# Kernel optimization log

Hardware: AMD Instinct MI355X
Metric: run time of the kernel (lower is better)

The kernel has to match this reference:

```python
import jax, jax.numpy as jnp
import numpy as np

B, L, C, H = 2, 2048, 1024, 16  # batches, tokens per batch, channels, heads


def _ln(x, eps=1e-6):
    # LayerNorm32: no affine, eps=1e-6, computed in fp32
    x32 = x.astype(jnp.float32)
    m = x32.mean(-1, keepdims=True)
    v = ((x32 - m) ** 2).mean(-1, keepdims=True)
    return ((x32 - m) * jax.lax.rsqrt(v + eps)).astype(x.dtype)


def setup_inputs() -> dict:
    key = jax.random.key(0)
    ks = jax.random.split(key, 8)
    s = 0.02
    return {
        "feats": jax.random.normal(ks[0], (B * L, C), jnp.float32),
        "mod": jax.random.normal(ks[1], (B, C), jnp.float32),
        "w_mod": jax.random.normal(ks[2], (C, 6 * C), jnp.float32) * s,
        "b_mod": jnp.zeros((6 * C,), jnp.float32),
        "w_qkv": jax.random.normal(ks[3], (C, 3 * C), jnp.float32) * s,
        "b_qkv": jnp.zeros((3 * C,), jnp.float32),
        "w_proj": jax.random.normal(ks[4], (C, C), jnp.float32) * s,
        "b_proj": jnp.zeros((C,), jnp.float32),
        "w_fc1": jax.random.normal(ks[5], (C, 4 * C), jnp.float32) * s,
        "b_fc1": jnp.zeros((4 * C,), jnp.float32),
        "w_fc2": jax.random.normal(ks[6], (4 * C, C), jnp.float32) * s,
        "b_fc2": jnp.zeros((C,), jnp.float32),
        "seq_len": L,
    }


def reference(feats, mod, w_mod, b_mod, w_qkv, b_qkv, w_proj, b_proj,
              w_fc1, b_fc1, w_fc2, b_fc2, seq_len):
    Bn, Cn = mod.shape
    Ln = seq_len
    Hn = H
    D = Cn // Hn

    # adaLN modulation: SiLU -> Linear(C, 6C), chunk into 6 [B, C] pieces
    m = jax.nn.silu(mod) @ w_mod + b_mod
    sh_a, sc_a, g_a, sh_m, sc_m, g_m = jnp.split(m, 6, axis=1)

    x = feats.reshape(Bn, Ln, Cn)

    # --- MSA branch ---
    h = _ln(x)
    h = h * (1.0 + sc_a[:, None]) + sh_a[:, None]
    qkv = h @ w_qkv + b_qkv  # [B, L, 3C]
    q, k, v = [t.reshape(Bn, Ln, Hn, D) for t in jnp.split(qkv, 3, axis=-1)]
    scores = jnp.einsum('bqhd,bkhd->bhqk', q, k) / jnp.sqrt(jnp.float32(D))
    a = jax.nn.softmax(scores, axis=-1)
    o = jnp.einsum('bhqk,bkhd->bqhd', a, v).reshape(Bn, Ln, Cn)
    o = o @ w_proj + b_proj
    x = x + o * g_a[:, None]

    # --- FFN branch ---
    h = _ln(x)
    h = h * (1.0 + sc_m[:, None]) + sh_m[:, None]
    h = jax.nn.gelu(h @ w_fc1 + b_fc1, approximate=False) @ w_fc2 + b_fc2
    x = x + h * g_m[:, None]

    return x.reshape(Bn * Ln, Cn)
```

## Files before the change

### kernel.cpp

```cpp
#include <hip/hip_runtime.h>
#include <hip/hip_bf16.h>
#include <math.h>

#define B_ 2
#define L_ 2048
#define C_ 1024
#define H_ 16
#define D_ 64

typedef __attribute__((ext_vector_type(8))) short short8;
typedef __attribute__((ext_vector_type(4))) float float4v;

__device__ inline short f2bs(float f) {
    union { __hip_bfloat16 h; short s; } u; u.h = __float2bfloat16(f); return u.s;
}

#define GL2LDS(gp, lp)                                                         \
    __builtin_amdgcn_global_load_lds(                                          \
        (const __attribute__((address_space(1))) void*)(gp),                   \
        (__attribute__((address_space(3))) void*)(lp), 16, 0, 0)

__global__ __launch_bounds__(256) void k_mod2(const float* __restrict__ mod,
                                              const float* __restrict__ w_mod,
                                              const float* __restrict__ b_mod,
                                              float* __restrict__ m_out) {
    __shared__ float a_s[2][256];
    const int t = threadIdx.x;
    const int seg = blockIdx.y;
    for (int i = t; i < 512; i += 256) {
        float a = mod[(i >> 8) * C_ + seg * 256 + (i & 255)];
        a_s[i >> 8][i & 255] = a / (1.f + __expf(-a));
    }
    __syncthreads();
    int j = blockIdx.x * 256 + t;
    float acc0 = (seg == 0) ? b_mod[j] : 0.f;
    float acc1 = acc0;
    for (int k = 0; k < 256; ++k) {
        float w = w_mod[(size_t)(seg * 256 + k) * (6 * C_) + j];
        acc0 += a_s[0][k] * w;
        acc1 += a_s[1][k] * w;
    }
    atomicAdd(&m_out[j], acc0);
    atomicAdd(&m_out[6 * C_ + j], acc1);
}

__global__ __launch_bounds__(256) void k_wt(const float* __restrict__ W,
                                            short* __restrict__ WT,
                                            int K, int N) {
    __shared__ short T[64][72];
    const int t = threadIdx.x;
    const int n0 = blockIdx.x * 64, k0 = blockIdx.y * 64;
    {
        int kr = t >> 2, nc = (t & 3) * 16;
        const float* src = W + (size_t)(k0 + kr) * N + n0 + nc;
#pragma unroll
        for (int j = 0; j < 16; ++j) T[kr][nc + j] = f2bs(src[j]);
    }
    __syncthreads();
    {
        int nr = t >> 2, kc = (t & 3) * 16;
        short8 o0, o1;
#pragma unroll
        for (int j = 0; j < 8; ++j) { o0[j] = T[kc + j][nr]; o1[j] = T[kc + 8 + j][nr]; }
        short* dst = WT + (size_t)(n0 + nr) * K + k0 + kc;
        *(short8*)dst = o0;
        *(short8*)(dst + 8) = o1;
    }
}

__global__ __launch_bounds__(256) void k_vt(const __hip_bfloat16* __restrict__ qkv,
                                            short* __restrict__ vt) {
    __shared__ short T[64][72];
    const int t = threadIdx.x;
    const int kt = blockIdx.x * 64;
    const int bh = blockIdx.y;
    const int h = bh & (H_ - 1), b = bh >> 4;
    const __hip_bfloat16* src = qkv + ((size_t)(b * L_ + kt)) * (3 * C_) + 2 * C_ + h * D_;
    {
        int kr = t >> 2, dg = (t & 3) * 16;
        const short8* s = (const short8*)(src + (size_t)kr * (3 * C_) + dg);
        *(short8*)&T[kr][dg] = s[0];
        *(short8*)&T[kr][dg + 8] = s[1];
    }
    __syncthreads();
    {
        int dr = t >> 2, kg = (t & 3) * 16;
        short8 o0, o1;
#pragma unroll
        for (int j = 0; j < 8; ++j) { o0[j] = T[kg + j][dr]; o1[j] = T[kg + 8 + j][dr]; }
        short* dst = vt + ((size_t)bh * D_ + dr) * L_ + kt + kg;
        *(short8*)dst = o0;
        *(short8*)(dst + 8) = o1;
    }
}

__global__ __launch_bounds__(256) void k_ln_mod(const float* __restrict__ x,
                                                const float* __restrict__ mvec,
                                                int off_sh, int off_sc,
                                                __hip_bfloat16* __restrict__ h_out) {
    int row = blockIdx.x;
    int b = row / L_;
    int t = threadIdx.x;
    float v[4];
    float s = 0.f, ss = 0.f;
#pragma unroll
    for (int i = 0; i < 4; ++i) {
        int c = t + i * 256;
        float val = x[(size_t)row * C_ + c];
        v[i] = val; s += val; ss += val * val;
    }
#pragma unroll
    for (int o = 32; o; o >>= 1) { s += __shfl_xor(s, o); ss += __shfl_xor(ss, o); }
    __shared__ float red[2][4];
    int wid = t >> 6, lane = t & 63;
    if (lane == 0) { red[0][wid] = s; red[1][wid] = ss; }
    __syncthreads();
    s  = red[0][0] + red[0][1] + red[0][2] + red[0][3];
    ss = red[1][0] + red[1][1] + red[1][2] + red[1][3];
    float mean = s * (1.f / C_);
    float var  = ss * (1.f / C_) - mean * mean;
    float rstd = rsqrtf(var + 1e-6f);
#pragma unroll
    for (int i = 0; i < 4; ++i) {
        int c = t + i * 256;
        float sc = mvec[b * (6 * C_) + off_sc + c];
        float sh = mvec[b * (6 * C_) + off_sh + c];
        float hn = (v[i] - mean) * rstd;
        h_out[(size_t)row * C_ + c] = __float2bfloat16(hn * (1.f + sc) + sh);
    }
}

__device__ inline void gemm_epilogue(float v, int m, int n, int N, int act, int emode,
                                     const float* __restrict__ gate,
                                     const float* __restrict__ resid_f,
                                     __hip_bfloat16* __restrict__ out_bf,
                                     float* __restrict__ out_f) {
    if (act == 1) v = 0.5f * v * (1.f + erff(v * 0.70710678118654752440f));
    if (emode == 2) {
        float g = gate[(m >> 11) * (6 * C_) + n];
        v = resid_f[(size_t)m * N + n] + v * g;
    }
    if (out_f) out_f[(size_t)m * N + n] = v;
    else       out_bf[(size_t)m * N + n] = __float2bfloat16(v);
}

template<int WM, int WN, int MI, int NI>
__global__ __launch_bounds__(256) void k_gemm_async(
        const __hip_bfloat16* __restrict__ A, int lda,
        const short* __restrict__ WT, int ldw,
        const float* __restrict__ bias,
        int M, int N, int K, int act, int emode,
        const float* __restrict__ gate,
        const float* __restrict__ resid_f,
        __hip_bfloat16* __restrict__ out_bf,
        float* __restrict__ out_f) {
    constexpr int BM = WM * MI * 16;
    constexpr int BN = WN * NI * 16;
    __shared__ __align__(16) short A_lds[BM * 64];
    __shared__ __align__(16) short B_lds[BN * 64];
    const int t = threadIdx.x;
    const int lane = t & 63;
    const int w = t >> 6;
    const int wm = w / WN, wn = w % WN;
    const int quad = lane >> 4, l16 = lane & 15;
    const int m0 = blockIdx.y * BM;
    const int n0 = blockIdx.x * BN;

    float4v acc[MI][NI] = {};

    for (int k0 = 0; k0 < K; k0 += 64) {
        __syncthreads();
#pragma unroll
        for (int rep = 0; rep < BM / 32; ++rep) {
            int p = rep * 256 + t;
            int row = p >> 3;
            int g = (p & 7) ^ (row & 7);
            const __hip_bfloat16* gp = A + (size_t)(m0 + row) * lda + k0 + g * 8;
            GL2LDS(gp, &A_lds[(rep * 256 + (t & ~63)) * 8]);
        }
#pragma unroll
        for (int rep = 0; rep < BN / 32; ++rep) {
            int p = rep * 256 + t;
            int row = p >> 3;
            int g = (p & 7) ^ (row & 7);
            const short* gp = WT + (size_t)(n0 + row) * ldw + k0 + g * 8;
            GL2LDS(gp, &B_lds[(rep * 256 + (t & ~63)) * 8]);
        }
        __syncthreads();
        short8 af[MI][2], bf[NI][2];
#pragma unroll
        for (int mi = 0; mi < MI; ++mi) {
            int r = wm * MI * 16 + mi * 16 + l16;
#pragma unroll
            for (int h = 0; h < 2; ++h)
                af[mi][h] = *(const short8*)(&A_lds[(r * 8 + ((h * 4 + quad) ^ (r & 7))) * 8]);
        }
#pragma unroll
        for (int ni = 0; ni < NI; ++ni) {
            int r = wn * NI * 16 + ni * 16 + l16;
#pragma unroll
            for (int h = 0; h < 2; ++h)
                bf[ni][h] = *(const short8*)(&B_lds[(r * 8 + ((h * 4 + quad) ^ (r & 7))) * 8]);
        }
#pragma unroll
        for (int h = 0; h < 2; ++h)
#pragma unroll
            for (int mi = 0; mi < MI; ++mi)
#pragma unroll
                for (int ni = 0; ni < NI; ++ni)
                    acc[mi][ni] = __builtin_amdgcn_mfma_f32_16x16x32_bf16(
                        af[mi][h], bf[ni][h], acc[mi][ni], 0, 0, 0);
    }

#pragma unroll
    for (int mi = 0; mi < MI; ++mi)
#pragma unroll
        for (int ni = 0; ni < NI; ++ni)
#pragma unroll
            for (int r = 0; r < 4; ++r) {
                int m = m0 + wm * MI * 16 + mi * 16 + quad * 4 + r;
                int n = n0 + wn * NI * 16 + ni * 16 + l16;
                float v = acc[mi][ni][r] + (bias ? bias[n] : 0.f);
                gemm_epilogue(v, m, n, N, act, emode, gate, resid_f, out_bf, out_f);
            }
}

__global__ __launch_bounds__(256) void k_attn(const __hip_bfloat16* __restrict__ qkv,
                                              const short* __restrict__ vt,
                                              __hip_bfloat16* __restrict__ o) {
    __shared__ short K_lds[64 * 72];
    __shared__ short V_lds[64 * 66];
    __shared__ short P_lds[4][16 * 68];
    const int t = threadIdx.x;
    const int lane = t & 63;
    const int w = t >> 6;
    const int quad = lane >> 4, l16 = lane & 15;

    const int blk = blockIdx.x;
    const int q_blk = (blk & 31) * 64;
    const int bh = blk >> 5;
    const int h = bh & (H_ - 1);
    const int b = bh >> 4;

    const size_t stride = 3 * C_;
    const __hip_bfloat16* base = qkv + (size_t)b * L_ * stride + h * D_;

    short8 qf[2];
    {
        const __hip_bfloat16* qrow = base + (size_t)(q_blk + w * 16 + l16) * stride;
        qf[0] = *(const short8*)(qrow + quad * 8);
        qf[1] = *(const short8*)(qrow + 32 + quad * 8);
    }
    short8 ones;
#pragma unroll
    for (int j = 0; j < 8; ++j) ones[j] = (short)0x3F80;

    float4v o_acc[4];
    float4v l_acc = (float4v){0.f, 0.f, 0.f, 0.f};
#pragma unroll
    for (int dt = 0; dt < 4; ++dt) o_acc[dt] = (float4v){0.f, 0.f, 0.f, 0.f};

    const int s_key = t >> 2;
    const int s_dg = (t & 3) * 16;
    const __hip_bfloat16* kg = base + C_;
    const short* vtb = vt + (size_t)bh * D_ * L_;

    for (int kt = 0; kt < L_; kt += 64) {
        __syncthreads();
        {
            const __hip_bfloat16* kr = kg + (size_t)(kt + s_key) * stride + s_dg;
            *(short8*)(&K_lds[s_key * 72 + s_dg]) = *(const short8*)(kr);
            *(short8*)(&K_lds[s_key * 72 + s_dg + 8]) = *(const short8*)(kr + 8);
        }
        {
            const short* vr = vtb + (size_t)s_key * L_ + kt + s_dg;
            *(short8*)(&V_lds[s_key * 66 + s_dg]) = *(const short8*)(vr);
            *(short8*)(&V_lds[s_key * 66 + s_dg + 8]) = *(const short8*)(vr + 8);
        }
        __syncthreads();

        float4v sacc[4];
#pragma unroll
        for (int kb = 0; kb < 4; ++kb) {
            sacc[kb] = (float4v){0.f, 0.f, 0.f, 0.f};
            short8 kf0 = *(const short8*)(&K_lds[(kb * 16 + l16) * 72 + quad * 8]);
            short8 kf1 = *(const short8*)(&K_lds[(kb * 16 + l16) * 72 + 32 + quad * 8]);
            sacc[kb] = __builtin_amdgcn_mfma_f32_16x16x32_bf16(qf[0], kf0, sacc[kb], 0, 0, 0);
            sacc[kb] = __builtin_amdgcn_mfma_f32_16x16x32_bf16(qf[1], kf1, sacc[kb], 0, 0, 0);
        }

#pragma unroll
        for (int r = 0; r < 4; ++r) {
            short* prow = &P_lds[w][(quad * 4 + r) * 68];
            prow[l16]      = f2bs(__expf(fmaf(sacc[0][r], 0.125f, -8.f)));
            prow[16 + l16] = f2bs(__expf(fmaf(sacc[1][r], 0.125f, -8.f)));
            prow[32 + l16] = f2bs(__expf(fmaf(sacc[2][r], 0.125f, -8.f)));
            prow[48 + l16] = f2bs(__expf(fmaf(sacc[3][r], 0.125f, -8.f)));
        }

        short8 pf0 = *(const short8*)(&P_lds[w][l16 * 68 + quad * 8]);
        short8 pf1 = *(const short8*)(&P_lds[w][l16 * 68 + 32 + quad * 8]);
        l_acc = __builtin_amdgcn_mfma_f32_16x16x32_bf16(pf0, ones, l_acc, 0, 0, 0);
        l_acc = __builtin_amdgcn_mfma_f32_16x16x32_bf16(pf1, ones, l_acc, 0, 0, 0);
#pragma unroll
        for (int dt = 0; dt < 4; ++dt) {
            short8 vf0 = *(const short8*)(&V_lds[(dt * 16 + l16) * 66 + quad * 8]);
            short8 vf1 = *(const short8*)(&V_lds[(dt * 16 + l16) * 66 + 32 + quad * 8]);
            o_acc[dt] = __builtin_amdgcn_mfma_f32_16x16x32_bf16(pf0, vf0, o_acc[dt], 0, 0, 0);
            o_acc[dt] = __builtin_amdgcn_mfma_f32_16x16x32_bf16(pf1, vf1, o_acc[dt], 0, 0, 0);
        }
    }

#pragma unroll
    for (int dt = 0; dt < 4; ++dt)
#pragma unroll
        for (int r = 0; r < 4; ++r) {
            int q = q_blk + w * 16 + quad * 4 + r;
            o[(size_t)(b * L_ + q) * C_ + h * D_ + dt * 16 + l16] =
                __float2bfloat16(o_acc[dt][r] / l_acc[r]);
        }
}

extern "C" void kernel_launch(void* const* d_in, const int* in_sizes, int n_in,
                              void* d_out, int out_size, void* d_ws, size_t ws_size,
                              hipStream_t stream) {
    const float* feats  = (const float*)d_in[0];
    const float* mod    = (const float*)d_in[1];
    const float* w_mod  = (const float*)d_in[2];
    const float* b_mod  = (const float*)d_in[3];
    const float* w_qkv  = (const float*)d_in[4];
    const float* b_qkv  = (const float*)d_in[5];
    const float* w_proj = (const float*)d_in[6];
    const float* b_proj = (const float*)d_in[7];
    const float* w_fc1  = (const float*)d_in[8];
    const float* b_fc1  = (const float*)d_in[9];
    const float* w_fc2  = (const float*)d_in[10];
    const float* b_fc2  = (const float*)d_in[11];

    const int M = B_ * L_;
    char* ws = (char*)d_ws;
    float* m_ws = (float*)ws;

    short* wqkvT  = (short*)(ws + 49152);
    short* wprojT = wqkvT + (size_t)3 * C_ * C_;
    short* wfc1T  = wprojT + (size_t)C_ * C_;
    short* wfc2T  = wfc1T + (size_t)4 * C_ * C_;
    char* slotB = (char*)(wfc2T + (size_t)4 * C_ * C_);
    __hip_bfloat16* qkv_ws = (__hip_bfloat16*)slotB;
    float* x1_ws           = (float*)slotB;
    __hip_bfloat16* slotA  = (__hip_bfloat16*)(slotB + (size_t)M * 3 * C_ * 2);
    __hip_bfloat16* hf_ws  = slotA + (size_t)M * C_;
    short* vt_ws           = (short*)hf_ws;

    k_wt<<<dim3(3 * C_ / 64, C_ / 64), 256, 0, stream>>>(w_qkv, wqkvT, C_, 3 * C_);
    k_wt<<<dim3(C_ / 64, C_ / 64), 256, 0, stream>>>(w_proj, wprojT, C_, C_);
    k_wt<<<dim3(4 * C_ / 64, C_ / 64), 256, 0, stream>>>(w_fc1, wfc1T, C_, 4 * C_);
    k_wt<<<dim3(C_ / 64, 4 * C_ / 64), 256, 0, stream>>>(w_fc2, wfc2T, 4 * C_, C_);
    hipMemsetAsync(m_ws, 0, 2 * 6 * C_ * sizeof(float), stream);
    k_mod2<<<dim3(24, 4), 256, 0, stream>>>(mod, w_mod, b_mod, m_ws);
    k_ln_mod<<<M, 256, 0, stream>>>(feats, m_ws, 0, 1024, slotA);
    k_gemm_async<2, 2, 4, 4><<<dim3(3 * C_ / 128, M / 128), 256, 0, stream>>>(
        slotA, C_, wqkvT, C_, b_qkv, M, 3 * C_, C_, 0, 0,
        nullptr, nullptr, qkv_ws, nullptr);
    k_vt<<<dim3(L_ / 64, B_ * H_), 256, 0, stream>>>(qkv_ws, vt_ws);
    k_attn<<<B_ * H_ * (L_ / 64), 256, 0, stream>>>(qkv_ws, vt_ws, slotA);
    k_gemm_async<4, 1, 2, 4><<<dim3(C_ / 64, M / 128), 256, 0, stream>>>(
        slotA, C_, wprojT, C_, b_proj, M, C_, C_, 0, 2,
        m_ws + 2 * C_, feats, nullptr, x1_ws);
    k_ln_mod<<<M, 256, 0, stream>>>(x1_ws, m_ws, 3 * C_, 4 * C_, slotA);
    k_gemm_async<2, 2, 4, 4><<<dim3(4 * C_ / 128, M / 128), 256, 0, stream>>>(
        slotA, C_, wfc1T, C_, b_fc1, M, 4 * C_, C_, 1, 0,
        nullptr, nullptr, hf_ws, nullptr);
    k_gemm_async<4, 1, 2, 4><<<dim3(C_ / 64, M / 128), 256, 0, stream>>>(
        hf_ws, 4 * C_, wfc2T, 4 * C_, b_fc2, M, C_, 4 * C_, 0, 2,
        m_ws + 5 * C_, x1_ws, nullptr, (float*)d_out);
}
```

Baseline: 519.7 us.

## Double-buffer attention K/V tiles with 512-thread blocks and merge weight transposes

Attention now uses 8 waves per block, so each block covers 128 queries and loads each K/V tile once for twice as many queries. K/V tiles are double-buffered in LDS, with the next tile prefetched into registers during compute, which leaves one barrier per iteration instead of two. The change also adds s_setprio around the MFMA sections, remaps block IDs so co-scheduled blocks share a head, and merges the four weight-transpose launches into one kernel. The costs are more LDS and registers per block and fewer blocks in the attention grid.

```diff
diff --git a/kernel.cpp b/kernel.cpp
--- a/kernel.cpp
+++ b/kernel.cpp
@@ -44,12 +44,21 @@
     atomicAdd(&m_out[6 * C_ + j], acc1);
 }
 
-__global__ __launch_bounds__(256) void k_wt(const float* __restrict__ W,
-                                            short* __restrict__ WT,
-                                            int K, int N) {
+__global__ __launch_bounds__(256) void k_wt_all(
+        const float* __restrict__ w_qkv, const float* __restrict__ w_proj,
+        const float* __restrict__ w_fc1, const float* __restrict__ w_fc2,
+        short* __restrict__ wqkvT, short* __restrict__ wprojT,
+        short* __restrict__ wfc1T, short* __restrict__ wfc2T) {
     __shared__ short T[64][72];
-    const int t = threadIdx.x;
-    const int n0 = blockIdx.x * 64, k0 = blockIdx.y * 64;
+    int id = blockIdx.x;
+    const float* W; short* WT; int K, N;
+    if (id < 768)       {             W = w_qkv;  WT = wqkvT;  K = C_;     N = 3 * C_; }
+    else if (id < 1024) { id -= 768;  W = w_proj; WT = wprojT; K = C_;     N = C_;     }
+    else if (id < 2048) { id -= 1024; W = w_fc1;  WT = wfc1T;  K = C_;     N = 4 * C_; }
+    else                { id -= 2048; W = w_fc2;  WT = wfc2T;  K = 4 * C_; N = C_;     }
+    const int nb = N >> 6;
+    const int n0 = (id % nb) * 64, k0 = (id / nb) * 64;
+    const int t = threadIdx.x;
     {
         int kr = t >> 2, nc = (t & 3) * 16;
         const float* src = W + (size_t)(k0 + kr) * N + n0 + nc;
@@ -225,20 +234,21 @@
             }
 }
 
-__global__ __launch_bounds__(256) void k_attn(const __hip_bfloat16* __restrict__ qkv,
+__global__ __launch_bounds__(512) void k_attn(const __hip_bfloat16* __restrict__ qkv,
                                               const short* __restrict__ vt,
                                               __hip_bfloat16* __restrict__ o) {
-    __shared__ short K_lds[64 * 72];
-    __shared__ short V_lds[64 * 66];
-    __shared__ short P_lds[4][16 * 68];
+    __shared__ __align__(16) short K_lds[2][64 * 72];
+    __shared__ __align__(16) short V_lds[2][64 * 72];
+    __shared__ __align__(16) short P_lds[8][16 * 72];
     const int t = threadIdx.x;
     const int lane = t & 63;
     const int w = t >> 6;
     const int quad = lane >> 4, l16 = lane & 15;
 
-    const int blk = blockIdx.x;
-    const int q_blk = (blk & 31) * 64;
-    const int bh = blk >> 5;
+    const int raw = blockIdx.x;
+    const int blk = (raw & 7) * 64 + (raw >> 3);
+    const int bh = blk >> 4;
+    const int q_blk = (blk & 15) * 128;
     const int h = bh & (H_ - 1);
     const int b = bh >> 4;
 
@@ -260,55 +270,64 @@
 #pragma unroll
     for (int dt = 0; dt < 4; ++dt) o_acc[dt] = (float4v){0.f, 0.f, 0.f, 0.f};
 
-    const int s_key = t >> 2;
-    const int s_dg = (t & 3) * 16;
+    const int s_row = t >> 3;
+    const int s_col = (t & 7) * 8;
     const __hip_bfloat16* kg = base + C_;
     const short* vtb = vt + (size_t)bh * D_ * L_;
 
-    for (int kt = 0; kt < L_; kt += 64) {
-        __syncthreads();
-        {
-            const __hip_bfloat16* kr = kg + (size_t)(kt + s_key) * stride + s_dg;
-            *(short8*)(&K_lds[s_key * 72 + s_dg]) = *(const short8*)(kr);
-            *(short8*)(&K_lds[s_key * 72 + s_dg + 8]) = *(const short8*)(kr + 8);
-        }
-        {
-            const short* vr = vtb + (size_t)s_key * L_ + kt + s_dg;
-            *(short8*)(&V_lds[s_key * 66 + s_dg]) = *(const short8*)(vr);
-            *(short8*)(&V_lds[s_key * 66 + s_dg + 8]) = *(const short8*)(vr + 8);
-        }
-        __syncthreads();
+    short8 kreg = *(const short8*)(kg + (size_t)s_row * stride + s_col);
+    short8 vreg = *(const short8*)(vtb + (size_t)s_row * L_ + s_col);
+    *(short8*)&K_lds[0][s_row * 72 + s_col] = kreg;
+    *(short8*)&V_lds[0][s_row * 72 + s_col] = vreg;
+    __syncthreads();
+
+    for (int kt = 0, cur = 0; kt < L_; kt += 64, cur ^= 1) {
+        const int nxt = kt + 64;
+        if (nxt < L_) {
+            kreg = *(const short8*)(kg + (size_t)(nxt + s_row) * stride + s_col);
+            vreg = *(const short8*)(vtb + (size_t)s_row * L_ + nxt + s_col);
+        }
 
         float4v sacc[4];
+        __builtin_amdgcn_s_setprio(1);
 #pragma unroll
         for (int kb = 0; kb < 4; ++kb) {
             sacc[kb] = (float4v){0.f, 0.f, 0.f, 0.f};
-            short8 kf0 = *(const short8*)(&K_lds[(kb * 16 + l16) * 72 + quad * 8]);
-            short8 kf1 = *(const short8*)(&K_lds[(kb * 16 + l16) * 72 + 32 + quad * 8]);
+            short8 kf0 = *(const short8*)(&K_lds[cur][(kb * 16 + l16) * 72 + quad * 8]);
+            short8 kf1 = *(const short8*)(&K_lds[cur][(kb * 16 + l16) * 72 + 32 + quad * 8]);
             sacc[kb] = __builtin_amdgcn_mfma_f32_16x16x32_bf16(qf[0], kf0, sacc[kb], 0, 0, 0);
             sacc[kb] = __builtin_amdgcn_mfma_f32_16x16x32_bf16(qf[1], kf1, sacc[kb], 0, 0, 0);
         }
+        __builtin_amdgcn_s_setprio(0);
 
 #pragma unroll
         for (int r = 0; r < 4; ++r) {
-            short* prow = &P_lds[w][(quad * 4 + r) * 68];
+            short* prow = &P_lds[w][(quad * 4 + r) * 72];
             prow[l16]      = f2bs(__expf(fmaf(sacc[0][r], 0.125f, -8.f)));
             prow[16 + l16] = f2bs(__expf(fmaf(sacc[1][r], 0.125f, -8.f)));
             prow[32 + l16] = f2bs(__expf(fmaf(sacc[2][r], 0.125f, -8.f)));
             prow[48 + l16] = f2bs(__expf(fmaf(sacc[3][r], 0.125f, -8.f)));
         }
 
-        short8 pf0 = *(const short8*)(&P_lds[w][l16 * 68 + quad * 8]);
-        short8 pf1 = *(const short8*)(&P_lds[w][l16 * 68 + 32 + quad * 8]);
+        short8 pf0 = *(const short8*)(&P_lds[w][l16 * 72 + quad * 8]);
+        short8 pf1 = *(const short8*)(&P_lds[w][l16 * 72 + 32 + quad * 8]);
+        __builtin_amdgcn_s_setprio(1);
         l_acc = __builtin_amdgcn_mfma_f32_16x16x32_bf16(pf0, ones, l_acc, 0, 0, 0);
         l_acc = __builtin_amdgcn_mfma_f32_16x16x32_bf16(pf1, ones, l_acc, 0, 0, 0);
 #pragma unroll
         for (int dt = 0; dt < 4; ++dt) {
-            short8 vf0 = *(const short8*)(&V_lds[(dt * 16 + l16) * 66 + quad * 8]);
-            short8 vf1 = *(const short8*)(&V_lds[(dt * 16 + l16) * 66 + 32 + quad * 8]);
+            short8 vf0 = *(const short8*)(&V_lds[cur][(dt * 16 + l16) * 72 + quad * 8]);
+            short8 vf1 = *(const short8*)(&V_lds[cur][(dt * 16 + l16) * 72 + 32 + quad * 8]);
             o_acc[dt] = __builtin_amdgcn_mfma_f32_16x16x32_bf16(pf0, vf0, o_acc[dt], 0, 0, 0);
             o_acc[dt] = __builtin_amdgcn_mfma_f32_16x16x32_bf16(pf1, vf1, o_acc[dt], 0, 0, 0);
         }
+        __builtin_amdgcn_s_setprio(0);
+
+        if (nxt < L_) {
+            *(short8*)&K_lds[cur ^ 1][s_row * 72 + s_col] = kreg;
+            *(short8*)&V_lds[cur ^ 1][s_row * 72 + s_col] = vreg;
+        }
+        __syncthreads();
     }
 
 #pragma unroll
@@ -352,10 +371,8 @@
     __hip_bfloat16* hf_ws  = slotA + (size_t)M * C_;
     short* vt_ws           = (short*)hf_ws;
 
-    k_wt<<<dim3(3 * C_ / 64, C_ / 64), 256, 0, stream>>>(w_qkv, wqkvT, C_, 3 * C_);
-    k_wt<<<dim3(C_ / 64, C_ / 64), 256, 0, stream>>>(w_proj, wprojT, C_, C_);
-    k_wt<<<dim3(4 * C_ / 64, C_ / 64), 256, 0, stream>>>(w_fc1, wfc1T, C_, 4 * C_);
-    k_wt<<<dim3(C_ / 64, 4 * C_ / 64), 256, 0, stream>>>(w_fc2, wfc2T, 4 * C_, C_);
+    k_wt_all<<<3072, 256, 0, stream>>>(w_qkv, w_proj, w_fc1, w_fc2,
+                                       wqkvT, wprojT, wfc1T, wfc2T);
     hipMemsetAsync(m_ws, 0, 2 * 6 * C_ * sizeof(float), stream);
     k_mod2<<<dim3(24, 4), 256, 0, stream>>>(mod, w_mod, b_mod, m_ws);
     k_ln_mod<<<M, 256, 0, stream>>>(feats, m_ws, 0, 1024, slotA);
@@ -363,7 +380,7 @@
         slotA, C_, wqkvT, C_, b_qkv, M, 3 * C_, C_, 0, 0,
         nullptr, nullptr, qkv_ws, nullptr);
     k_vt<<<dim3(L_ / 64, B_ * H_), 256, 0, stream>>>(qkv_ws, vt_ws);
-    k_attn<<<B_ * H_ * (L_ / 64), 256, 0, stream>>>(qkv_ws, vt_ws, slotA);
+    k_attn<<<B_ * H_ * (L_ / 128), 512, 0, stream>>>(qkv_ws, vt_ws, slotA);
     k_gemm_async<4, 1, 2, 4><<<dim3(C_ / 64, M / 128), 256, 0, stream>>>(
         slotA, C_, wprojT, C_, b_proj, M, C_, C_, 0, 2,
         m_ws + 2 * C_, feats, nullptr, x1_ws);
```

New measurement: 490.1 us. -5.7%, faster.
